# Kernel optimization log

Measured on AMD Instinct MI355X. Metric: run time of the kernel, lower is better.

Reference implementation:

```python
import jax, jax.numpy as jnp
import numpy as np

N_NODES = 100000
N_EDGES = 20000  # hyperedges
NNZ = 800000
D = 128


def setup_inputs() -> dict:
    key = jax.random.key(0)
    ks = jax.random.split(key, 10)
    X = jax.random.normal(ks[0], (N_NODES, D), dtype=jnp.float32)
    X0 = jax.random.normal(ks[1], (N_NODES, D), dtype=jnp.float32)
    degE = jax.random.uniform(ks[2], (N_EDGES, 1), dtype=jnp.float32)
    degV = jax.random.uniform(ks[3], (N_NODES, 1), dtype=jnp.float32)
    alpha = jax.random.uniform(ks[4], (1,), dtype=jnp.float32)
    beta = jax.random.uniform(ks[5], (1,), dtype=jnp.float32)
    W_w = jax.random.normal(ks[6], (D, D), dtype=jnp.float32) / np.sqrt(D)
    g1_src = jax.random.randint(ks[7], (NNZ,), 0, N_NODES, dtype=jnp.int64 if jax.config.read('jax_enable_x64') else jnp.int32)
    g1_dst = jax.random.randint(ks[8], (NNZ,), 0, N_EDGES)
    g2_src = jax.random.randint(ks[9], (NNZ,), 0, N_EDGES)
    g2_dst = jax.random.randint(jax.random.fold_in(key, 99), (NNZ,), 0, N_NODES)
    return {"X": X, "X0": X0, "degE": degE, "degV": degV, "alpha": alpha,
            "beta": beta, "W_w": W_w, "g1_src": g1_src, "g1_dst": g1_dst,
            "g2_src": g2_src, "g2_dst": g2_dst}


def reference(X, X0, degE, degV, alpha, beta, W_w, g1_src, g1_dst, g2_src, g2_dst):
    n_edges = degE.shape[0]
    n_nodes = degV.shape[0]
    a = alpha[0]
    b = beta[0]
    # copy_u_sum(g1, X): gather node rows, scatter-sum into hyperedges
    Xe = jax.ops.segment_sum(X[g1_src], g1_dst, num_segments=n_edges)  # [E, D]
    Xe = Xe * degE
    # copy_u_sum(g2, Xe): gather hyperedge rows, scatter-sum into nodes
    Xv = jax.ops.segment_sum(Xe[g2_src], g2_dst, num_segments=n_nodes)  # [N, D]
    Xv = Xv * degV
    # GCNII-style initial residual + identity mapping
    Xi = (1.0 - a) * Xv + a * X0
    out = (1.0 - b) * Xi + b * (Xi @ W_w.T)  # Linear(bias=False)
    return out
```

## Files before the change

### kernel.cpp

```cpp
#include <hip/hip_runtime.h>

#define DD 128
#define SCAN_CHUNK 2048
#define PAD1 16
#define PAD2 8

typedef __attribute__((ext_vector_type(8))) short bf16x8;
typedef __attribute__((ext_vector_type(4))) short bf16x4;
typedef __attribute__((ext_vector_type(4))) float f32x4;

__device__ __forceinline__ short f2bf(float f) {
    union { float f; unsigned u; } x; x.f = f;
    unsigned r = x.u + 0x7FFF + ((x.u >> 16) & 1);
    return (short)(r >> 16);
}
__device__ __forceinline__ float bf2f(short h) {
    union { float f; unsigned u; } x;
    x.u = ((unsigned)(unsigned short)h) << 16;
    return x.f;
}

__global__ __launch_bounds__(256)
void k_hist1(const int* __restrict__ g1d, int* __restrict__ cnt1p,
             int* __restrict__ rank1, int nnz, int no,
             const float* __restrict__ W, const float* __restrict__ betaP,
             short* __restrict__ Mbf) {
    if (blockIdx.x < 8) {
        int gid = blockIdx.x * 256 + threadIdx.x;
        if (gid >= DD * DD / 8) return;
        int c  = gid >> 4;
        int k0 = (gid & 15) << 3;
        float b = betaP[0], ib = 1.0f - b;
        const float* p = W + c * DD + k0;
        float4 lo = *(const float4*)p, hi = *(const float4*)(p + 4);
        float v[8] = {lo.x, lo.y, lo.z, lo.w, hi.x, hi.y, hi.z, hi.w};
        bf16x8 t;
        #pragma unroll
        for (int j = 0; j < 8; ++j) {
            float m = b * v[j] + ((k0 + j) == c ? ib : 0.0f);
            t[j] = f2bf(m);
        }
        *(bf16x8*)(Mbf + (size_t)c * DD + k0) = t;
        return;
    }
    int q = (blockIdx.x - 8) * 256 + threadIdx.x;
    if (q >= no) return;
    int i = q << 3;
    if (i + 8 <= nnz) {
        int4 d0 = *(const int4*)(g1d + i);
        int4 d1 = *(const int4*)(g1d + i + 4);
        int r0 = atomicAdd(&cnt1p[d0.x * PAD1], 1);
        int r1 = atomicAdd(&cnt1p[d0.y * PAD1], 1);
        int r2 = atomicAdd(&cnt1p[d0.z * PAD1], 1);
        int r3 = atomicAdd(&cnt1p[d0.w * PAD1], 1);
        int r4 = atomicAdd(&cnt1p[d1.x * PAD1], 1);
        int r5 = atomicAdd(&cnt1p[d1.y * PAD1], 1);
        int r6 = atomicAdd(&cnt1p[d1.z * PAD1], 1);
        int r7 = atomicAdd(&cnt1p[d1.w * PAD1], 1);
        *(int4*)(rank1 + i)     = make_int4(r0, r1, r2, r3);
        *(int4*)(rank1 + i + 4) = make_int4(r4, r5, r6, r7);
    } else {
        for (; i < nnz; ++i) rank1[i] = atomicAdd(&cnt1p[g1d[i] * PAD1], 1);
    }
}

__global__ __launch_bounds__(256)
void k_scan_blocks(const int* __restrict__ cnt, int* __restrict__ off,
                   int* __restrict__ bsum, int n, int str) {
    __shared__ int sh[256];
    const int tid = threadIdx.x;
    const int base = blockIdx.x * SCAN_CHUNK + tid * 8;
    int v[8];
    int s = 0;
    #pragma unroll
    for (int j = 0; j < 8; ++j) {
        int idx = base + j;
        v[j] = (idx < n) ? cnt[(size_t)idx * str] : 0;
        s += v[j];
    }
    sh[tid] = s;
    __syncthreads();
    for (int d = 1; d < 256; d <<= 1) {
        int y = (tid >= d) ? sh[tid - d] : 0;
        __syncthreads();
        sh[tid] += y;
        __syncthreads();
    }
    int incl = sh[tid];
    int run = incl - s;
    #pragma unroll
    for (int j = 0; j < 8; ++j) {
        int idx = base + j;
        if (idx < n) off[idx] = run;
        run += v[j];
    }
    if (tid == 255) bsum[blockIdx.x] = incl;
}

__global__ __launch_bounds__(256)
void k_scan_add(int* __restrict__ off, const int* __restrict__ bsum,
                int n, int nnz) {
    int gid = blockIdx.x * 256 + threadIdx.x;
    if (gid == 0) off[n] = nnz;
    if (gid >= n) return;
    int chunk = gid >> 11;
    int p = 0;
    for (int i = 0; i < chunk; ++i) p += bsum[i];
    off[gid] += p;
}

__global__ __launch_bounds__(256)
void k_fill(const int* __restrict__ dst, const int* __restrict__ src,
            const int* __restrict__ off, const int* __restrict__ rank,
            int* __restrict__ out, int nnz, int str) {
    int q = blockIdx.x * 256 + threadIdx.x;
    int i = q << 2;
    if (i + 4 <= nnz) {
        int4 d = *(const int4*)(dst + i);
        int4 s = *(const int4*)(src + i);
        int4 r = *(const int4*)(rank + i);
        int o0 = off[d.x];
        int o1 = off[d.y];
        int o2 = off[d.z];
        int o3 = off[d.w];
        out[o0 + r.x] = s.x;
        out[o1 + r.y] = s.y;
        out[o2 + r.z] = s.z;
        out[o3 + r.w] = s.w;
    } else {
        for (; i < nnz; ++i) out[off[dst[i]] + rank[i]] = src[i];
    }
    (void)str;
}

__global__ __launch_bounds__(256)
void k_h2_egather(const int* __restrict__ g2d, int* __restrict__ cnt2p,
                  int* __restrict__ rank2, int nnz, int no, int H,
                  const float* __restrict__ X, const int* __restrict__ off1,
                  const int* __restrict__ srcs1, const float* __restrict__ degE,
                  short* __restrict__ XeBF, int n_edges) {
    if (blockIdx.x < H) {
        int q = blockIdx.x * 256 + threadIdx.x;
        if (q >= no) return;
        int i = q << 3;
        if (i + 8 <= nnz) {
            int4 d0 = *(const int4*)(g2d + i);
            int4 d1 = *(const int4*)(g2d + i + 4);
            int r0 = atomicAdd(&cnt2p[d0.x * PAD2], 1);
            int r1 = atomicAdd(&cnt2p[d0.y * PAD2], 1);
            int r2 = atomicAdd(&cnt2p[d0.z * PAD2], 1);
            int r3 = atomicAdd(&cnt2p[d0.w * PAD2], 1);
            int r4 = atomicAdd(&cnt2p[d1.x * PAD2], 1);
            int r5 = atomicAdd(&cnt2p[d1.y * PAD2], 1);
            int r6 = atomicAdd(&cnt2p[d1.z * PAD2], 1);
            int r7 = atomicAdd(&cnt2p[d1.w * PAD2], 1);
            *(int4*)(rank2 + i)     = make_int4(r0, r1, r2, r3);
            *(int4*)(rank2 + i + 4) = make_int4(r4, r5, r6, r7);
        } else {
            for (; i < nnz; ++i) rank2[i] = atomicAdd(&cnt2p[g2d[i] * PAD2], 1);
        }
        return;
    }
    int gid = (blockIdx.x - H) * 256 + threadIdx.x;
    int e = gid >> 5;
    if (e >= n_edges) return;
    int k = (gid & 31) << 2;
    int beg = off1[e], end = off1[e + 1];
    float4 acc0 = {0, 0, 0, 0}, acc1 = {0, 0, 0, 0};
    float4 acc2 = {0, 0, 0, 0}, acc3 = {0, 0, 0, 0};
    int j = beg;
    for (; j + 8 <= end; j += 8) {
        int s0 = srcs1[j + 0];
        int s1 = srcs1[j + 1];
        int s2 = srcs1[j + 2];
        int s3 = srcs1[j + 3];
        int s4 = srcs1[j + 4];
        int s5 = srcs1[j + 5];
        int s6 = srcs1[j + 6];
        int s7 = srcs1[j + 7];
        float4 v0 = *(const float4*)(X + (size_t)s0 * DD + k);
        float4 v1 = *(const float4*)(X + (size_t)s1 * DD + k);
        float4 v2 = *(const float4*)(X + (size_t)s2 * DD + k);
        float4 v3 = *(const float4*)(X + (size_t)s3 * DD + k);
        float4 v4 = *(const float4*)(X + (size_t)s4 * DD + k);
        float4 v5 = *(const float4*)(X + (size_t)s5 * DD + k);
        float4 v6 = *(const float4*)(X + (size_t)s6 * DD + k);
        float4 v7 = *(const float4*)(X + (size_t)s7 * DD + k);
        acc0.x += v0.x; acc0.y += v0.y; acc0.z += v0.z; acc0.w += v0.w;
        acc1.x += v1.x; acc1.y += v1.y; acc1.z += v1.z; acc1.w += v1.w;
        acc2.x += v2.x; acc2.y += v2.y; acc2.z += v2.z; acc2.w += v2.w;
        acc3.x += v3.x; acc3.y += v3.y; acc3.z += v3.z; acc3.w += v3.w;
        acc0.x += v4.x; acc0.y += v4.y; acc0.z += v4.z; acc0.w += v4.w;
        acc1.x += v5.x; acc1.y += v5.y; acc1.z += v5.z; acc1.w += v5.w;
        acc2.x += v6.x; acc2.y += v6.y; acc2.z += v6.z; acc2.w += v6.w;
        acc3.x += v7.x; acc3.y += v7.y; acc3.z += v7.z; acc3.w += v7.w;
    }
    for (; j < end; ++j) {
        int s = srcs1[j];
        float4 v = *(const float4*)(X + (size_t)s * DD + k);
        acc0.x += v.x; acc0.y += v.y; acc0.z += v.z; acc0.w += v.w;
    }
    float f = degE[e];
    bf16x4 ob;
    ob[0] = f2bf(f * ((acc0.x + acc1.x) + (acc2.x + acc3.x)));
    ob[1] = f2bf(f * ((acc0.y + acc1.y) + (acc2.y + acc3.y)));
    ob[2] = f2bf(f * ((acc0.z + acc1.z) + (acc2.z + acc3.z)));
    ob[3] = f2bf(f * ((acc0.w + acc1.w) + (acc2.w + acc3.w)));
    *(bf16x4*)(XeBF + (size_t)e * DD + k) = ob;
}

__global__ __launch_bounds__(256)
void k_node_gather(const short* __restrict__ XeBF, const int* __restrict__ off,
                   const int* __restrict__ srcs, const float* __restrict__ degV,
                   const float* __restrict__ X0, const float* __restrict__ alphaP,
                   float* __restrict__ Xi, int n_nodes) {
    int gid = blockIdx.x * 256 + threadIdx.x;
    int v = gid >> 5;
    if (v >= n_nodes) return;
    int k = (gid & 31) << 2;
    int beg = off[v], end = off[v + 1];
    float4 acc0 = {0, 0, 0, 0}, acc1 = {0, 0, 0, 0};
    int j = beg;
    for (; j + 4 <= end; j += 4) {
        int s0 = srcs[j + 0];
        int s1 = srcs[j + 1];
        int s2 = srcs[j + 2];
        int s3 = srcs[j + 3];
        bf16x4 h0 = *(const bf16x4*)(XeBF + (size_t)s0 * DD + k);
        bf16x4 h1 = *(const bf16x4*)(XeBF + (size_t)s1 * DD + k);
        bf16x4 h2 = *(const bf16x4*)(XeBF + (size_t)s2 * DD + k);
        bf16x4 h3 = *(const bf16x4*)(XeBF + (size_t)s3 * DD + k);
        acc0.x += bf2f(h0[0]); acc0.y += bf2f(h0[1]); acc0.z += bf2f(h0[2]); acc0.w += bf2f(h0[3]);
        acc1.x += bf2f(h1[0]); acc1.y += bf2f(h1[1]); acc1.z += bf2f(h1[2]); acc1.w += bf2f(h1[3]);
        acc0.x += bf2f(h2[0]); acc0.y += bf2f(h2[1]); acc0.z += bf2f(h2[2]); acc0.w += bf2f(h2[3]);
        acc1.x += bf2f(h3[0]); acc1.y += bf2f(h3[1]); acc1.z += bf2f(h3[2]); acc1.w += bf2f(h3[3]);
    }
    for (; j < end; ++j) {
        int s = srcs[j];
        bf16x4 h = *(const bf16x4*)(XeBF + (size_t)s * DD + k);
        acc0.x += bf2f(h[0]); acc0.y += bf2f(h[1]); acc0.z += bf2f(h[2]); acc0.w += bf2f(h[3]);
    }
    float a = alphaP[0];
    float f = (1.0f - a) * degV[v];
    float4 x0 = *(const float4*)(X0 + (size_t)v * DD + k);
    float4 o;
    o.x = f * (acc0.x + acc1.x) + a * x0.x;
    o.y = f * (acc0.y + acc1.y) + a * x0.y;
    o.z = f * (acc0.z + acc1.z) + a * x0.z;
    o.w = f * (acc0.w + acc1.w) + a * x0.w;
    *(float4*)(Xi + (size_t)v * DD + k) = o;
}

__global__ __launch_bounds__(256)
void k_gemm_mfma(float* xio, const short* __restrict__ Mbf, int n_rows) {
    const int lane = threadIdx.x & 63;
    const int wid  = threadIdx.x >> 6;
    const int m16  = lane & 15;
    const int quad = lane >> 4;
    const int kq   = quad * 8;

    const int strip = blockIdx.x * 4 + wid;
    const int row0 = strip * 16;
    if (row0 >= n_rows) return;

    int arow = row0 + m16;
    if (arow >= n_rows) arow = n_rows - 1;
    const float* xr = xio + (size_t)arow * DD;

    bf16x8 af[4];
    #pragma unroll
    for (int kf = 0; kf < 4; ++kf) {
        const float* p = xr + kf * 32 + kq;
        float4 lo = *(const float4*)p;
        float4 hi = *(const float4*)(p + 4);
        bf16x8 t;
        t[0] = f2bf(lo.x); t[1] = f2bf(lo.y); t[2] = f2bf(lo.z); t[3] = f2bf(lo.w);
        t[4] = f2bf(hi.x); t[5] = f2bf(hi.y); t[6] = f2bf(hi.z); t[7] = f2bf(hi.w);
        af[kf] = t;
    }

    #pragma unroll
    for (int nt = 0; nt < 8; ++nt) {
        const short* mr = Mbf + (size_t)(nt * 16 + m16) * DD + kq;
        f32x4 acc = {0.f, 0.f, 0.f, 0.f};
        #pragma unroll
        for (int kf = 0; kf < 4; ++kf) {
            bf16x8 bfrag = *(const bf16x8*)(mr + kf * 32);
            acc = __builtin_amdgcn_mfma_f32_16x16x32_bf16(af[kf], bfrag, acc, 0, 0, 0);
        }
        const int col = nt * 16 + m16;
        #pragma unroll
        for (int r = 0; r < 4; ++r) {
            int row = row0 + quad * 4 + r;
            if (row < n_rows)
                xio[(size_t)row * DD + col] = acc[r];
        }
    }
}

extern "C" void kernel_launch(void* const* d_in, const int* in_sizes, int n_in,
                              void* d_out, int out_size, void* d_ws, size_t ws_size,
                              hipStream_t stream) {
    const float* X     = (const float*)d_in[0];
    const float* X0    = (const float*)d_in[1];
    const float* degE  = (const float*)d_in[2];
    const float* degV  = (const float*)d_in[3];
    const float* alpha = (const float*)d_in[4];
    const float* beta  = (const float*)d_in[5];
    const float* W     = (const float*)d_in[6];
    const int*   g1s   = (const int*)d_in[7];
    const int*   g1d   = (const int*)d_in[8];
    const int*   g2s   = (const int*)d_in[9];
    const int*   g2d   = (const int*)d_in[10];
    float* out = (float*)d_out;

    const int n_nodes = in_sizes[3];
    const int n_edges = in_sizes[2];
    const int nnz     = in_sizes[7];

    int*   wsi   = (int*)d_ws;
    short* XeBF  = (short*)d_ws;
    size_t o     = (size_t)n_edges * DD / 2;
    int*   rank1 = wsi + o;
    int*   rank2 = rank1;
    o += nnz;
    int*   off1  = wsi + o;          o += n_edges + 1;
    int*   off2  = wsi + o;          o += n_nodes + 1;
    size_t srcs_base = o;
    int*   srcs1 = wsi + o;          o += nnz;
    int*   srcs2 = wsi + o;          o += nnz;
    int*   bsum  = wsi + o;          o += 64;
    short* Mbf   = (short*)(wsi + o); o += DD * DD / 2;
    int*   cnt1p = wsi + srcs_base;
    int*   cnt2p = wsi + srcs_base + nnz;

    hipMemsetAsync(cnt1p, 0, 2 * (size_t)nnz * sizeof(int), stream);

    const int nb1 = (n_edges + SCAN_CHUNK - 1) / SCAN_CHUNK;
    const int nb2 = (n_nodes + SCAN_CHUNK - 1) / SCAN_CHUNK;
    const int no  = (nnz + 7) / 8;
    const int hb  = (no + 255) / 256;
    const int nq  = (nnz + 3) / 4;
    const int qb  = (nq + 255) / 256;

    k_hist1<<<8 + hb, 256, 0, stream>>>(g1d, cnt1p, rank1, nnz, no, W, beta, Mbf);
    k_scan_blocks<<<nb1, 256, 0, stream>>>(cnt1p, off1, bsum, n_edges, PAD1);
    k_scan_add<<<(n_edges + 255) / 256, 256, 0, stream>>>(off1, bsum, n_edges, nnz);
    k_fill<<<qb, 256, 0, stream>>>(g1d, g1s, off1, rank1, srcs1, nnz, PAD1);

    const int egb = (n_edges * 32 + 255) / 256;
    k_h2_egather<<<hb + egb, 256, 0, stream>>>(g2d, cnt2p, rank2, nnz, no, hb,
                                               X, off1, srcs1, degE, XeBF, n_edges);

    k_scan_blocks<<<nb2, 256, 0, stream>>>(cnt2p, off2, bsum, n_nodes, PAD2);
    k_scan_add<<<(n_nodes + 255) / 256, 256, 0, stream>>>(off2, bsum, n_nodes, nnz);
    k_fill<<<qb, 256, 0, stream>>>(g2d, g2s, off2, rank2, srcs2, nnz, PAD2);

    k_node_gather<<<(n_nodes * 32 + 255) / 256, 256, 0, stream>>>(
        XeBF, off2, srcs2, degV, X0, alpha, out, n_nodes);

    const int nstrips = (n_nodes + 15) / 16;
    k_gemm_mfma<<<(nstrips + 3) / 4, 256, 0, stream>>>(out, Mbf, n_nodes);
}
```

Baseline: 391.6 us.

## Convert X to fp16 upfront and gather half-precision rows for hyperedge sums

```diff
diff --git a/kernel.cpp b/kernel.cpp
--- a/kernel.cpp
+++ b/kernel.cpp
@@ -5,62 +5,70 @@
 #define PAD1 16
 #define PAD2 8
 
-typedef __attribute__((ext_vector_type(8))) short bf16x8;
-typedef __attribute__((ext_vector_type(4))) short bf16x4;
+typedef __attribute__((ext_vector_type(8))) _Float16 f16x8;
+typedef __attribute__((ext_vector_type(4))) _Float16 f16x4;
 typedef __attribute__((ext_vector_type(4))) float f32x4;
 
-__device__ __forceinline__ short f2bf(float f) {
-    union { float f; unsigned u; } x; x.f = f;
-    unsigned r = x.u + 0x7FFF + ((x.u >> 16) & 1);
-    return (short)(r >> 16);
-}
-__device__ __forceinline__ float bf2f(short h) {
-    union { float f; unsigned u; } x;
-    x.u = ((unsigned)(unsigned short)h) << 16;
-    return x.f;
-}
-
 __global__ __launch_bounds__(256)
 void k_hist1(const int* __restrict__ g1d, int* __restrict__ cnt1p,
-             int* __restrict__ rank1, int nnz, int no,
+             int* __restrict__ rank1, int nnz, int no, int hb,
              const float* __restrict__ W, const float* __restrict__ betaP,
-             short* __restrict__ Mbf) {
-    if (blockIdx.x < 8) {
-        int gid = blockIdx.x * 256 + threadIdx.x;
+             _Float16* __restrict__ Mh,
+             const float* __restrict__ X, _Float16* __restrict__ Xh, int nx) {
+    const int b = blockIdx.x;
+    if (b < hb) {
+        int q = b * 256 + threadIdx.x;
+        if (q >= no) return;
+        int i = q << 3;
+        if (i + 8 <= nnz) {
+            int4 d0 = *(const int4*)(g1d + i);
+            int4 d1 = *(const int4*)(g1d + i + 4);
+            int r0 = atomicAdd(&cnt1p[d0.x * PAD1], 1);
+            int r1 = atomicAdd(&cnt1p[d0.y * PAD1], 1);
+            int r2 = atomicAdd(&cnt1p[d0.z * PAD1], 1);
+            int r3 = atomicAdd(&cnt1p[d0.w * PAD1], 1);
+            int r4 = atomicAdd(&cnt1p[d1.x * PAD1], 1);
+            int r5 = atomicAdd(&cnt1p[d1.y * PAD1], 1);
+            int r6 = atomicAdd(&cnt1p[d1.z * PAD1], 1);
+            int r7 = atomicAdd(&cnt1p[d1.w * PAD1], 1);
+            *(int4*)(rank1 + i)     = make_int4(r0, r1, r2, r3);
+            *(int4*)(rank1 + i + 4) = make_int4(r4, r5, r6, r7);
+        } else {
+            for (; i < nnz; ++i) rank1[i] = atomicAdd(&cnt1p[g1d[i] * PAD1], 1);
+        }
+        return;
+    }
+    if (b < hb + 8) {
+        int gid = (b - hb) * 256 + threadIdx.x;
         if (gid >= DD * DD / 8) return;
         int c  = gid >> 4;
         int k0 = (gid & 15) << 3;
-        float b = betaP[0], ib = 1.0f - b;
+        float bb = betaP[0], ib = 1.0f - bb;
         const float* p = W + c * DD + k0;
         float4 lo = *(const float4*)p, hi = *(const float4*)(p + 4);
         float v[8] = {lo.x, lo.y, lo.z, lo.w, hi.x, hi.y, hi.z, hi.w};
-        bf16x8 t;
+        f16x8 t;
         #pragma unroll
         for (int j = 0; j < 8; ++j) {
-            float m = b * v[j] + ((k0 + j) == c ? ib : 0.0f);
-            t[j] = f2bf(m);
-        }
-        *(bf16x8*)(Mbf + (size_t)c * DD + k0) = t;
+            float m = bb * v[j] + ((k0 + j) == c ? ib : 0.0f);
+            t[j] = (_Float16)m;
+        }
+        *(f16x8*)(Mh + (size_t)c * DD + k0) = t;
         return;
     }
-    int q = (blockIdx.x - 8) * 256 + threadIdx.x;
-    if (q >= no) return;
-    int i = q << 3;
-    if (i + 8 <= nnz) {
-        int4 d0 = *(const int4*)(g1d + i);
-        int4 d1 = *(const int4*)(g1d + i + 4);
-        int r0 = atomicAdd(&cnt1p[d0.x * PAD1], 1);
-        int r1 = atomicAdd(&cnt1p[d0.y * PAD1], 1);
-        int r2 = atomicAdd(&cnt1p[d0.z * PAD1], 1);
-        int r3 = atomicAdd(&cnt1p[d0.w * PAD1], 1);
-        int r4 = atomicAdd(&cnt1p[d1.x * PAD1], 1);
-        int r5 = atomicAdd(&cnt1p[d1.y * PAD1], 1);
-        int r6 = atomicAdd(&cnt1p[d1.z * PAD1], 1);
-        int r7 = atomicAdd(&cnt1p[d1.w * PAD1], 1);
-        *(int4*)(rank1 + i)     = make_int4(r0, r1, r2, r3);
-        *(int4*)(rank1 + i + 4) = make_int4(r4, r5, r6, r7);
+    int gid = (b - hb - 8) * 256 + threadIdx.x;
+    int i = gid << 3;
+    if (i + 8 <= nx) {
+        float4 lo = *(const float4*)(X + i);
+        float4 hi = *(const float4*)(X + i + 4);
+        f16x8 t;
+        t[0] = (_Float16)lo.x; t[1] = (_Float16)lo.y;
+        t[2] = (_Float16)lo.z; t[3] = (_Float16)lo.w;
+        t[4] = (_Float16)hi.x; t[5] = (_Float16)hi.y;
+        t[6] = (_Float16)hi.z; t[7] = (_Float16)hi.w;
+        *(f16x8*)(Xh + i) = t;
     } else {
-        for (; i < nnz; ++i) rank1[i] = atomicAdd(&cnt1p[g1d[i] * PAD1], 1);
+        for (; i < nx; ++i) Xh[i] = (_Float16)X[i];
     }
 }
 
@@ -112,7 +120,7 @@
 __global__ __launch_bounds__(256)
 void k_fill(const int* __restrict__ dst, const int* __restrict__ src,
             const int* __restrict__ off, const int* __restrict__ rank,
-            int* __restrict__ out, int nnz, int str) {
+            int* __restrict__ out, int nnz) {
     int q = blockIdx.x * 256 + threadIdx.x;
     int i = q << 2;
     if (i + 4 <= nnz) {
@@ -130,15 +138,14 @@
     } else {
         for (; i < nnz; ++i) out[off[dst[i]] + rank[i]] = src[i];
     }
-    (void)str;
 }
 
 __global__ __launch_bounds__(256)
 void k_h2_egather(const int* __restrict__ g2d, int* __restrict__ cnt2p,
                   int* __restrict__ rank2, int nnz, int no, int H,
-                  const float* __restrict__ X, const int* __restrict__ off1,
+                  const _Float16* __restrict__ Xh, const int* __restrict__ off1,
                   const int* __restrict__ srcs1, const float* __restrict__ degE,
-                  short* __restrict__ XeBF, int n_edges) {
+                  _Float16* __restrict__ XeH, int n_edges) {
     if (blockIdx.x < H) {
         int q = blockIdx.x * 256 + threadIdx.x;
         if (q >= no) return;
@@ -162,12 +169,12 @@
         return;
     }
     int gid = (blockIdx.x - H) * 256 + threadIdx.x;
-    int e = gid >> 5;
+    int e = gid >> 4;
     if (e >= n_edges) return;
-    int k = (gid & 31) << 2;
+    int k = (gid & 15) << 3;
     int beg = off1[e], end = off1[e + 1];
-    float4 acc0 = {0, 0, 0, 0}, acc1 = {0, 0, 0, 0};
-    float4 acc2 = {0, 0, 0, 0}, acc3 = {0, 0, 0, 0};
+    float a0[8] = {0, 0, 0, 0, 0, 0, 0, 0};
+    float a1[8] = {0, 0, 0, 0, 0, 0, 0, 0};
     int j = beg;
     for (; j + 8 <= end; j += 8) {
         int s0 = srcs1[j + 0];
@@ -178,39 +185,40 @@
         int s5 = srcs1[j + 5];
         int s6 = srcs1[j + 6];
         int s7 = srcs1[j + 7];
-        float4 v0 = *(const float4*)(X + (size_t)s0 * DD + k);
-        float4 v1 = *(const float4*)(X + (size_t)s1 * DD + k);
-        float4 v2 = *(const float4*)(X + (size_t)s2 * DD + k);
-        float4 v3 = *(const float4*)(X + (size_t)s3 * DD + k);
-        float4 v4 = *(const float4*)(X + (size_t)s4 * DD + k);
-        float4 v5 = *(const float4*)(X + (size_t)s5 * DD + k);
-        float4 v6 = *(const float4*)(X + (size_t)s6 * DD + k);
-        float4 v7 = *(const float4*)(X + (size_t)s7 * DD + k);
-        acc0.x += v0.x; acc0.y += v0.y; acc0.z += v0.z; acc0.w += v0.w;
-        acc1.x += v1.x; acc1.y += v1.y; acc1.z += v1.z; acc1.w += v1.w;
-        acc2.x += v2.x; acc2.y += v2.y; acc2.z += v2.z; acc2.w += v2.w;
-        acc3.x += v3.x; acc3.y += v3.y; acc3.z += v3.z; acc3.w += v3.w;
-        acc0.x += v4.x; acc0.y += v4.y; acc0.z += v4.z; acc0.w += v4.w;
-        acc1.x += v5.x; acc1.y += v5.y; acc1.z += v5.z; acc1.w += v5.w;
-        acc2.x += v6.x; acc2.y += v6.y; acc2.z += v6.z; acc2.w += v6.w;
-        acc3.x += v7.x; acc3.y += v7.y; acc3.z += v7.z; acc3.w += v7.w;
+        f16x8 v0 = *(const f16x8*)(Xh + (size_t)s0 * DD + k);
+        f16x8 v1 = *(const f16x8*)(Xh + (size_t)s1 * DD + k);
+        f16x8 v2 = *(const f16x8*)(Xh + (size_t)s2 * DD + k);
+        f16x8 v3 = *(const f16x8*)(Xh + (size_t)s3 * DD + k);
+        f16x8 v4 = *(const f16x8*)(Xh + (size_t)s4 * DD + k);
+        f16x8 v5 = *(const f16x8*)(Xh + (size_t)s5 * DD + k);
+        f16x8 v6 = *(const f16x8*)(Xh + (size_t)s6 * DD + k);
+        f16x8 v7 = *(const f16x8*)(Xh + (size_t)s7 * DD + k);
+        #pragma unroll
+        for (int t = 0; t < 8; ++t) {
+            a0[t] += (float)v0[t] + (float)v2[t];
+            a1[t] += (float)v1[t] + (float)v3[t];
+        }
+        #pragma unroll
+        for (int t = 0; t < 8; ++t) {
+            a0[t] += (float)v4[t] + (float)v6[t];
+            a1[t] += (float)v5[t] + (float)v7[t];
+        }
     }
     for (; j < end; ++j) {
         int s = srcs1[j];
-        float4 v = *(const float4*)(X + (size_t)s * DD + k);
-        acc0.x += v.x; acc0.y += v.y; acc0.z += v.z; acc0.w += v.w;
+        f16x8 v = *(const f16x8*)(Xh + (size_t)s * DD + k);
+        #pragma unroll
+        for (int t = 0; t < 8; ++t) a0[t] += (float)v[t];
     }
     float f = degE[e];
-    bf16x4 ob;
-    ob[0] = f2bf(f * ((acc0.x + acc1.x) + (acc2.x + acc3.x)));
-    ob[1] = f2bf(f * ((acc0.y + acc1.y) + (acc2.y + acc3.y)));
-    ob[2] = f2bf(f * ((acc0.z + acc1.z) + (acc2.z + acc3.z)));
-    ob[3] = f2bf(f * ((acc0.w + acc1.w) + (acc2.w + acc3.w)));
-    *(bf16x4*)(XeBF + (size_t)e * DD + k) = ob;
-}
-
-__global__ __launch_bounds__(256)
-void k_node_gather(const short* __restrict__ XeBF, const int* __restrict__ off,
+    f16x8 ob;
+    #pragma unroll
+    for (int t = 0; t < 8; ++t) ob[t] = (_Float16)(f * (a0[t] + a1[t]));
+    *(f16x8*)(XeH + (size_t)e * DD + k) = ob;
+}
+
+__global__ __launch_bounds__(256)
+void k_node_gather(const _Float16* __restrict__ XeH, const int* __restrict__ off,
                    const int* __restrict__ srcs, const float* __restrict__ degV,
                    const float* __restrict__ X0, const float* __restrict__ alphaP,
                    float* __restrict__ Xi, int n_nodes) {
@@ -226,19 +234,19 @@
         int s1 = srcs[j + 1];
         int s2 = srcs[j + 2];
         int s3 = srcs[j + 3];
-        bf16x4 h0 = *(const bf16x4*)(XeBF + (size_t)s0 * DD + k);
-        bf16x4 h1 = *(const bf16x4*)(XeBF + (size_t)s1 * DD + k);
-        bf16x4 h2 = *(const bf16x4*)(XeBF + (size_t)s2 * DD + k);
-        bf16x4 h3 = *(const bf16x4*)(XeBF + (size_t)s3 * DD + k);
-        acc0.x += bf2f(h0[0]); acc0.y += bf2f(h0[1]); acc0.z += bf2f(h0[2]); acc0.w += bf2f(h0[3]);
-        acc1.x += bf2f(h1[0]); acc1.y += bf2f(h1[1]); acc1.z += bf2f(h1[2]); acc1.w += bf2f(h1[3]);
-        acc0.x += bf2f(h2[0]); acc0.y += bf2f(h2[1]); acc0.z += bf2f(h2[2]); acc0.w += bf2f(h2[3]);
-        acc1.x += bf2f(h3[0]); acc1.y += bf2f(h3[1]); acc1.z += bf2f(h3[2]); acc1.w += bf2f(h3[3]);
+        f16x4 h0 = *(const f16x4*)(XeH + (size_t)s0 * DD + k);
+        f16x4 h1 = *(const f16x4*)(XeH + (size_t)s1 * DD + k);
+        f16x4 h2 = *(const f16x4*)(XeH + (size_t)s2 * DD + k);
+        f16x4 h3 = *(const f16x4*)(XeH + (size_t)s3 * DD + k);
+        acc0.x += (float)h0[0]; acc0.y += (float)h0[1]; acc0.z += (float)h0[2]; acc0.w += (float)h0[3];
+        acc1.x += (float)h1[0]; acc1.y += (float)h1[1]; acc1.z += (float)h1[2]; acc1.w += (float)h1[3];
+        acc0.x += (float)h2[0]; acc0.y += (float)h2[1]; acc0.z += (float)h2[2]; acc0.w += (float)h2[3];
+        acc1.x += (float)h3[0]; acc1.y += (float)h3[1]; acc1.z += (float)h3[2]; acc1.w += (float)h3[3];
     }
     for (; j < end; ++j) {
         int s = srcs[j];
-        bf16x4 h = *(const bf16x4*)(XeBF + (size_t)s * DD + k);
-        acc0.x += bf2f(h[0]); acc0.y += bf2f(h[1]); acc0.z += bf2f(h[2]); acc0.w += bf2f(h[3]);
+        f16x4 h = *(const f16x4*)(XeH + (size_t)s * DD + k);
+        acc0.x += (float)h[0]; acc0.y += (float)h[1]; acc0.z += (float)h[2]; acc0.w += (float)h[3];
     }
     float a = alphaP[0];
     float f = (1.0f - a) * degV[v];
@@ -252,7 +260,7 @@
 }
 
 __global__ __launch_bounds__(256)
-void k_gemm_mfma(float* xio, const short* __restrict__ Mbf, int n_rows) {
+void k_gemm_mfma(float* xio, const _Float16* __restrict__ Mh, int n_rows) {
     const int lane = threadIdx.x & 63;
     const int wid  = threadIdx.x >> 6;
     const int m16  = lane & 15;
@@ -267,26 +275,28 @@
     if (arow >= n_rows) arow = n_rows - 1;
     const float* xr = xio + (size_t)arow * DD;
 
-    bf16x8 af[4];
+    f16x8 af[4];
     #pragma unroll
     for (int kf = 0; kf < 4; ++kf) {
         const float* p = xr + kf * 32 + kq;
         float4 lo = *(const float4*)p;
         float4 hi = *(const float4*)(p + 4);
-        bf16x8 t;
-        t[0] = f2bf(lo.x); t[1] = f2bf(lo.y); t[2] = f2bf(lo.z); t[3] = f2bf(lo.w);
-        t[4] = f2bf(hi.x); t[5] = f2bf(hi.y); t[6] = f2bf(hi.z); t[7] = f2bf(hi.w);
+        f16x8 t;
+        t[0] = (_Float16)lo.x; t[1] = (_Float16)lo.y;
+        t[2] = (_Float16)lo.z; t[3] = (_Float16)lo.w;
+        t[4] = (_Float16)hi.x; t[5] = (_Float16)hi.y;
+        t[6] = (_Float16)hi.z; t[7] = (_Float16)hi.w;
         af[kf] = t;
     }
 
     #pragma unroll
     for (int nt = 0; nt < 8; ++nt) {
-        const short* mr = Mbf + (size_t)(nt * 16 + m16) * DD + kq;
+        const _Float16* mr = Mh + (size_t)(nt * 16 + m16) * DD + kq;
         f32x4 acc = {0.f, 0.f, 0.f, 0.f};
         #pragma unroll
         for (int kf = 0; kf < 4; ++kf) {
-            bf16x8 bfrag = *(const bf16x8*)(mr + kf * 32);
-            acc = __builtin_amdgcn_mfma_f32_16x16x32_bf16(af[kf], bfrag, acc, 0, 0, 0);
+            f16x8 bfrag = *(const f16x8*)(mr + kf * 32);
+            acc = __builtin_amdgcn_mfma_f32_16x16x32_f16(af[kf], bfrag, acc, 0, 0, 0);
         }
         const int col = nt * 16 + m16;
         #pragma unroll
@@ -317,9 +327,10 @@
     const int n_nodes = in_sizes[3];
     const int n_edges = in_sizes[2];
     const int nnz     = in_sizes[7];
+    const int nx      = n_nodes * DD;
 
     int*   wsi   = (int*)d_ws;
-    short* XeBF  = (short*)d_ws;
+    _Float16* XeH = (_Float16*)d_ws;
     size_t o     = (size_t)n_edges * DD / 2;
     int*   rank1 = wsi + o;
     int*   rank2 = rank1;
@@ -330,9 +341,10 @@
     int*   srcs1 = wsi + o;          o += nnz;
     int*   srcs2 = wsi + o;          o += nnz;
     int*   bsum  = wsi + o;          o += 64;
-    short* Mbf   = (short*)(wsi + o); o += DD * DD / 2;
+    _Float16* Mh = (_Float16*)(wsi + o); o += DD * DD / 2;
     int*   cnt1p = wsi + srcs_base;
     int*   cnt2p = wsi + srcs_base + nnz;
+    _Float16* Xh = (_Float16*)d_out;
 
     hipMemsetAsync(cnt1p, 0, 2 * (size_t)nnz * sizeof(int), stream);
 
@@ -340,25 +352,27 @@
     const int nb2 = (n_nodes + SCAN_CHUNK - 1) / SCAN_CHUNK;
     const int no  = (nnz + 7) / 8;
     const int hb  = (no + 255) / 256;
+    const int cb  = (nx / 8 + 255) / 256;
     const int nq  = (nnz + 3) / 4;
     const int qb  = (nq + 255) / 256;
 
-    k_hist1<<<8 + hb, 256, 0, stream>>>(g1d, cnt1p, rank1, nnz, no, W, beta, Mbf);
+    k_hist1<<<hb + 8 + cb, 256, 0, stream>>>(g1d, cnt1p, rank1, nnz, no, hb,
+                                             W, beta, Mh, X, Xh, nx);
     k_scan_blocks<<<nb1, 256, 0, stream>>>(cnt1p, off1, bsum, n_edges, PAD1);
     k_scan_add<<<(n_edges + 255) / 256, 256, 0, stream>>>(off1, bsum, n_edges, nnz);
-    k_fill<<<qb, 256, 0, stream>>>(g1d, g1s, off1, rank1, srcs1, nnz, PAD1);
-
-    const int egb = (n_edges * 32 + 255) / 256;
+    k_fill<<<qb, 256, 0, stream>>>(g1d, g1s, off1, rank1, srcs1, nnz);
+
+    const int egb = (n_edges * 16 + 255) / 256;
     k_h2_egather<<<hb + egb, 256, 0, stream>>>(g2d, cnt2p, rank2, nnz, no, hb,
-                                               X, off1, srcs1, degE, XeBF, n_edges);
+                                               Xh, off1, srcs1, degE, XeH, n_edges);
 
     k_scan_blocks<<<nb2, 256, 0, stream>>>(cnt2p, off2, bsum, n_nodes, PAD2);
     k_scan_add<<<(n_nodes + 255) / 256, 256, 0, stream>>>(off2, bsum, n_nodes, nnz);
-    k_fill<<<qb, 256, 0, stream>>>(g2d, g2s, off2, rank2, srcs2, nnz, PAD2);
+    k_fill<<<qb, 256, 0, stream>>>(g2d, g2s, off2, rank2, srcs2, nnz);
 
     k_node_gather<<<(n_nodes * 32 + 255) / 256, 256, 0, stream>>>(
-        XeBF, off2, srcs2, degV, X0, alpha, out, n_nodes);
+        XeH, off2, srcs2, degV, X0, alpha, out, n_nodes);
 
     const int nstrips = (n_nodes + 15) / 16;
-    k_gemm_mfma<<<(nstrips + 3) / 4, 256, 0, stream>>>(out, Mbf, n_nodes);
-}
+    k_gemm_mfma<<<(nstrips + 3) / 4, 256, 0, stream>>>(out, Mh, n_nodes);
+}
```

After: 374.8 us. 1.04x faster.
